# Kernel tuning notes

Measured on AMD Instinct MI355X. Metric: run time of the kernel, lower is better.

Reference implementation:

```python
import jax, jax.numpy as jnp
import numpy as np

B, L, T_BASE = 8192, 512, 4
T = T_BASE + 2            # +START, +STOP
START, STOP = T_BASE, T_BASE + 1
NEG = -10000.0


def setup_inputs() -> dict:
    key = jax.random.key(0)
    k1, k2, k3, k4 = jax.random.split(key, 4)
    feats = jax.random.normal(k1, (B, L, T), dtype=jnp.float32)
    trans = jax.random.normal(k2, (T, T), dtype=jnp.float32)
    # transitions[START, :] = -10000 (never transition out of nothing into START... i.e. into START)
    trans = trans.at[START, :].set(NEG)
    # transitions[:, STOP] = -10000 (never transition from STOP)
    trans = trans.at[:, STOP].set(NEG)
    tags = jax.random.randint(k3, (B, L), 0, T_BASE, dtype=jnp.int64)
    seq_lengths = jax.random.randint(k4, (B,), 1, L + 1, dtype=jnp.int32)
    return {"feats": feats, "transitions": trans, "tags": tags, "seq_lengths": seq_lengths}


def _crf_nll(feats, trans, tags, seq_lengths):
    # feats: [B, L, T], trans: [T, T] with trans[next, prev], tags: [B, L], seq_lengths: [B]
    mask = (jnp.arange(L)[None, :] < seq_lengths[:, None])  # [B, L] bool

    # ---- forward algorithm (log partition), batched over B, scanned over time ----
    init_alpha = jnp.full((feats.shape[0], T), NEG, dtype=feats.dtype).at[:, START].set(0.0)

    def step(alpha, xs):
        feat_t, mask_t = xs  # [B, T], [B]
        # scores[b, next, prev] = alpha[b, prev] + trans[next, prev]
        scores = alpha[:, None, :] + trans[None, :, :]
        new_alpha = jax.nn.logsumexp(scores, axis=-1) + feat_t  # [B, T]
        alpha = jnp.where(mask_t[:, None], new_alpha, alpha)
        return alpha, None

    feats_t = jnp.swapaxes(feats, 0, 1)   # [L, B, T]
    mask_t = jnp.swapaxes(mask, 0, 1)     # [L, B]
    alpha, _ = jax.lax.scan(step, init_alpha, (feats_t, mask_t))
    log_z = jax.nn.logsumexp(alpha + trans[STOP][None, :], axis=-1)  # [B]

    # ---- gold path score, fully vectorized ----
    tags32 = tags.astype(jnp.int32)
    start_col = jnp.full((tags32.shape[0], 1), START, dtype=jnp.int32)
    tags_ext = jnp.concatenate([start_col, tags32], axis=1)  # [B, L+1]
    trans_sc = trans[tags_ext[:, 1:], tags_ext[:, :-1]]       # [B, L]
    emit_sc = jnp.take_along_axis(feats, tags32[..., None], axis=2)[..., 0]  # [B, L]
    maskf = mask.astype(feats.dtype)
    gold = jnp.sum(maskf * (trans_sc + emit_sc), axis=1)      # [B]
    last_tag = jnp.take_along_axis(tags32, (seq_lengths[:, None] - 1).astype(jnp.int32), axis=1)[:, 0]
    gold = gold + trans[STOP, last_tag]

    return jnp.sum(log_z - gold) / feats.shape[0]


def reference(feats, transitions, tags, seq_lengths):
    return _crf_nll(feats, transitions, tags, seq_lengths)
```

## Files before the change

kernel.cpp:

```cpp
#include <hip/hip_runtime.h>


#define BB 8192
#define LL 512
#define LN2F 0.69314718055994530942f

__device__ __forceinline__ float uniformf(float x) {
    return __uint_as_float(__builtin_amdgcn_readfirstlane(__float_as_uint(x)));
}

#define RENORM16(P, MEX)                                                \
  do {                                                                  \
    float m_ = fmaxf(P[0], P[1]);                                       \
    _Pragma("unroll") for (int z_ = 2; z_ < 16; ++z_) m_ = fmaxf(m_, P[z_]); \
    const int ee_ = (int)((__float_as_uint(m_) >> 23) & 255) - 127;     \
    const float sc_ = __uint_as_float((unsigned)(127 - ee_) << 23);     \
    _Pragma("unroll") for (int z_ = 0; z_ < 16; ++z_) P[z_] *= sc_;     \
    MEX += ee_;                                                         \
  } while (0)

#define STEP(ABS, F0, F1, F2, F3, TG, PV)                               \
  do {                                                                  \
    const bool act_ = (ABS) < len;                                      \
    const float f0_=(F0), f1_=(F1), f2_=(F2), f3_=(F3);                 \
    const float fe0_=__expf(f0_), fe1_=__expf(f1_);                     \
    const float fe2_=__expf(f2_), fe3_=__expf(f3_);                     \
    _Pragma("unroll")                                                   \
    for (int j = 0; j < 4; ++j) {                                       \
      const float c0_=P[0*4+j], c1_=P[1*4+j], c2_=P[2*4+j], c3_=P[3*4+j]; \
      const float t0_ = fmaf(E[0], c0_, fmaf(E[1], c1_, fmaf(E[2], c2_, E[3] *c3_))); \
      const float t1_ = fmaf(E[4], c0_, fmaf(E[5], c1_, fmaf(E[6], c2_, E[7] *c3_))); \
      const float t2_ = fmaf(E[8], c0_, fmaf(E[9], c1_, fmaf(E[10],c2_, E[11]*c3_))); \
      const float t3_ = fmaf(E[12],c0_, fmaf(E[13],c1_, fmaf(E[14],c2_, E[15]*c3_))); \
      P[0*4+j] = act_ ? fe0_*t0_ : P[0*4+j];                            \
      P[1*4+j] = act_ ? fe1_*t1_ : P[1*4+j];                            \
      P[2*4+j] = act_ ? fe2_*t2_ : P[2*4+j];                            \
      P[3*4+j] = act_ ? fe3_*t3_ : P[3*4+j];                            \
    }                                                                   \
    const float lut_ = sT[(TG) * 6 + (PV)];                             \
    const float em_  = ((TG) & 2) ? (((TG) & 1) ? f3_ : f2_)            \
                                  : (((TG) & 1) ? f1_ : f0_);           \
    gold += act_ ? (lut_ + em_) : 0.f;                                  \
  } while (0)

#define TGAT(S)  ((int)((tpk >> (2*(S))) & 3u))
#define STEPE(S) STEP(base+(S), F0[(S)/2].x, F0[(S)/2].y, F0[(S)/2].z, F0[(S)/2].w, TGAT(S), TGAT((S)-1))
#define STEPO(S) STEP(base+(S), F1[(S)/2].x, F1[(S)/2].y, F2[(S)/2].x, F2[(S)/2].y, TGAT(S), TGAT((S)-1))

__global__ __launch_bounds__(256, 4) void crf_tree(
    const float* __restrict__ feats,
    const float* __restrict__ trans,
    const int*   __restrict__ tags,
    const int*   __restrict__ lens,
    float* __restrict__ partials)
{
    __shared__ float sT[36];

    const int tid  = threadIdx.x;
    const int lane = tid & 63;
    const int wv   = tid >> 6;
    const int g    = lane >> 5;
    const int c    = lane & 31;
    const int b    = blockIdx.x * 8 + wv * 2 + g;

    if (tid < 36) sT[tid] = trans[tid];
    __syncthreads();

    float E[16], e4[4], e5[4];
    #pragma unroll
    for (int i = 0; i < 16; ++i)
        E[i] = uniformf(__expf(sT[(i >> 2) * 6 + (i & 3)]));
    #pragma unroll
    for (int i = 0; i < 4; ++i) {
        e4[i] = uniformf(__expf(sT[i * 6 + 4]));
        e5[i] = uniformf(__expf(sT[30 + i]));
    }

    const int len  = lens[b];
    const int base = c * 16;
    const bool seg0 = (c == 0);

    const float* fp  = feats + (size_t)b * (LL * 6) + (size_t)base * 6;
    const int*   tbp = tags  + (size_t)b * LL + base;
    const int pv0 = seg0 ? 4 : (tbp[-1] & 3);

    float4 F0[8]; float2 F1[8], F2[8];
    #pragma unroll
    for (int p = 0; p < 8; ++p) {
        const float* q = fp + p * 12;
        F0[p] = *(const float4*)(q);
        F1[p] = *(const float2*)(q + 6);
        F2[p] = *(const float2*)(q + 8);
    }
    unsigned tpk = 0;
    #pragma unroll
    for (int q = 0; q < 4; ++q) {
        const int4 t = *(const int4*)(tbp + q * 4);
        tpk |= (unsigned)(t.x & 3) << (2*(q*4+0));
        tpk |= (unsigned)(t.y & 3) << (2*(q*4+1));
        tpk |= (unsigned)(t.z & 3) << (2*(q*4+2));
        tpk |= (unsigned)(t.w & 3) << (2*(q*4+3));
    }

    float P[16];
    #pragma unroll
    for (int z = 0; z < 16; ++z) P[z] = (z % 5 == 0) ? 1.f : 0.f;
    int   mex  = 0;
    float gold = 0.f;

    {
        const bool act_ = base < len;
        const float f0_=F0[0].x, f1_=F0[0].y, f2_=F0[0].z, f3_=F0[0].w;
        const float fe0_=__expf(f0_), fe1_=__expf(f1_);
        const float fe2_=__expf(f2_), fe3_=__expf(f3_);
        #pragma unroll
        for (int j = 0; j < 4; ++j) {
            const float u0 = seg0 ? e4[0] : E[0*4+j];
            const float u1 = seg0 ? e4[1] : E[1*4+j];
            const float u2 = seg0 ? e4[2] : E[2*4+j];
            const float u3 = seg0 ? e4[3] : E[3*4+j];
            P[0*4+j] = act_ ? fe0_*u0 : P[0*4+j];
            P[1*4+j] = act_ ? fe1_*u1 : P[1*4+j];
            P[2*4+j] = act_ ? fe2_*u2 : P[2*4+j];
            P[3*4+j] = act_ ? fe3_*u3 : P[3*4+j];
        }
        const int t0 = TGAT(0);
        const float lut_ = sT[t0 * 6 + pv0];
        const float em_  = (t0 & 2) ? ((t0 & 1) ? f3_ : f2_)
                                    : ((t0 & 1) ? f1_ : f0_);
        gold += act_ ? (lut_ + em_) : 0.f;
    }
    STEPO(1);  STEPE(2);  STEPO(3);  RENORM16(P, mex);
    STEPE(4);  STEPO(5);  STEPE(6);  STEPO(7);  RENORM16(P, mex);
    STEPE(8);  STEPO(9);  STEPE(10); STEPO(11); RENORM16(P, mex);
    STEPE(12); STEPO(13); STEPE(14); STEPO(15); RENORM16(P, mex);

    {
        const unsigned dl = (unsigned)(len - 1 - base);
        if (dl < 16u) gold += sT[30 + (int)((tpk >> (2*dl)) & 3u)];
    }

    #pragma unroll
    for (int k = 1; k <= 8; k <<= 1) {
        float Q[16];
        #pragma unroll
        for (int z = 0; z < 16; ++z) Q[z] = __shfl_down(P[z], k, 32);
        const int mq = __shfl_down(mex, k, 32);
        float N[16];
        #pragma unroll
        for (int i = 0; i < 4; ++i)
            #pragma unroll
            for (int j = 0; j < 4; ++j)
                N[i*4+j] = fmaf(Q[i*4+0], P[0*4+j], fmaf(Q[i*4+1], P[1*4+j],
                           fmaf(Q[i*4+2], P[2*4+j], Q[i*4+3] * P[3*4+j])));
        #pragma unroll
        for (int z = 0; z < 16; ++z) P[z] = N[z];
        mex += mq;
        if (k == 2 || k == 8) RENORM16(P, mex);
    }

    float al0, al1, al2, al3;
    {
        float Q[16];
        #pragma unroll
        for (int z = 0; z < 16; ++z) Q[z] = __shfl_down(P[z], 16, 32);
        const int mq = __shfl_down(mex, 16, 32);
        al0 = fmaf(Q[0], P[0], fmaf(Q[1], P[4], fmaf(Q[2], P[8], Q[3] *P[12])));
        al1 = fmaf(Q[4], P[0], fmaf(Q[5], P[4], fmaf(Q[6], P[8], Q[7] *P[12])));
        al2 = fmaf(Q[8], P[0], fmaf(Q[9], P[4], fmaf(Q[10],P[8], Q[11]*P[12])));
        al3 = fmaf(Q[12],P[0], fmaf(Q[13],P[4], fmaf(Q[14],P[8], Q[15]*P[12])));
        mex += mq;
    }

    #pragma unroll
    for (int k = 1; k <= 16; k <<= 1)
        gold += __shfl_xor(gold, k, 32);

    const float dot = fmaf(e5[0], al0, fmaf(e5[1], al1,
                      fmaf(e5[2], al2, e5[3] * al3)));
    const float logz = fmaf((float)mex, LN2F, __logf(dot));
    if (c == 0)
        partials[b] = logz - gold;
}

__global__ __launch_bounds__(256) void k_reduce(const float* __restrict__ partials,
                                               float* __restrict__ out)
{
    __shared__ float sh[256];
    const int t = threadIdx.x;
    float s = 0.f;
    #pragma unroll
    for (int j = 0; j < 32; ++j) s += partials[t + 256 * j];
    sh[t] = s;
    __syncthreads();
    #pragma unroll
    for (int d = 128; d > 0; d >>= 1) {
        if (t < d) sh[t] += sh[t + d];
        __syncthreads();
    }
    if (t == 0) out[0] = sh[0] * (1.0f / 8192.0f);
}

extern "C" void kernel_launch(void* const* d_in, const int* in_sizes, int n_in,
                              void* d_out, int out_size, void* d_ws, size_t ws_size,
                              hipStream_t stream) {
    const float* feats = (const float*)d_in[0];
    const float* trans = (const float*)d_in[1];
    const int*   tags  = (const int*)d_in[2];
    const int*   lens  = (const int*)d_in[3];
    float* out = (float*)d_out;
    float* partials = (float*)d_ws;

    crf_tree<<<BB / 8, 256, 0, stream>>>(feats, trans, tags, lens, partials);
    k_reduce<<<1, 256, 0, stream>>>(partials, out);
}
```

Before: 32.16 us.

## Size per-wave segment length to the wave's max sequence length

Each wave now sizes its segment length from the larger of its two sequences' lengths instead of a fixed 16 steps per lane. Feature and tag loads, and the scan steps beyond that length, are skipped behind wave-uniform guards. This cuts HBM traffic and ALU work for masked-out timesteps. The cost is extra branching and a less regular unrolled schedule, with renormalization now tied to the pair count.

After: 32.18 us. No clear change (+0.0%).

```diff
diff --git a/kernel.cpp b/kernel.cpp
--- a/kernel.cpp
+++ b/kernel.cpp
@@ -19,9 +19,9 @@
     MEX += ee_;                                                         \
   } while (0)
 
-#define STEP(ABS, F0, F1, F2, F3, TG, PV)                               \
+#define STEP(S, F0, F1, F2, F3, TG, PV)                                 \
   do {                                                                  \
-    const bool act_ = (ABS) < len;                                      \
+    const bool act_ = (base + (S)) < len;                               \
     const float f0_=(F0), f1_=(F1), f2_=(F2), f3_=(F3);                 \
     const float fe0_=__expf(f0_), fe1_=__expf(f1_);                     \
     const float fe2_=__expf(f2_), fe3_=__expf(f3_);                     \
@@ -44,8 +44,8 @@
   } while (0)
 
 #define TGAT(S)  ((int)((tpk >> (2*(S))) & 3u))
-#define STEPE(S) STEP(base+(S), F0[(S)/2].x, F0[(S)/2].y, F0[(S)/2].z, F0[(S)/2].w, TGAT(S), TGAT((S)-1))
-#define STEPO(S) STEP(base+(S), F1[(S)/2].x, F1[(S)/2].y, F2[(S)/2].x, F2[(S)/2].y, TGAT(S), TGAT((S)-1))
+#define STEPE(S) STEP((S), F0[(S)/2].x, F0[(S)/2].y, F0[(S)/2].z, F0[(S)/2].w, TGAT(S), TGAT((S)-1))
+#define STEPO(S) STEP((S), F1[(S)/2].x, F1[(S)/2].y, F2[(S)/2].x, F2[(S)/2].y, TGAT(S), TGAT((S)-1))
 
 __global__ __launch_bounds__(256, 4) void crf_tree(
     const float* __restrict__ feats,
@@ -76,8 +76,12 @@
         e5[i] = uniformf(__expf(sT[30 + i]));
     }
 
-    const int len  = lens[b];
-    const int base = c * 16;
+    const int len = lens[b];
+
+    const int wmax  = max(len, __shfl_xor(len, 32, 64));
+    const int seg2  = __builtin_amdgcn_readfirstlane(((wmax + 31) >> 5) + 1) & ~1;
+    const int npair = __builtin_amdgcn_readfirstlane(seg2 >> 1);
+    const int base  = c * seg2;
     const bool seg0 = (c == 0);
 
     const float* fp  = feats + (size_t)b * (LL * 6) + (size_t)base * 6;
@@ -86,21 +90,23 @@
 
     float4 F0[8]; float2 F1[8], F2[8];
     #pragma unroll
-    for (int p = 0; p < 8; ++p) {
-        const float* q = fp + p * 12;
-        F0[p] = *(const float4*)(q);
-        F1[p] = *(const float2*)(q + 6);
-        F2[p] = *(const float2*)(q + 8);
-    }
+    for (int p = 0; p < 8; ++p)
+        if (p < npair) {
+            const float* q = fp + p * 12;
+            F0[p] = *(const float4*)(q);
+            F1[p] = *(const float2*)(q + 6);
+            F2[p] = *(const float2*)(q + 8);
+        }
     unsigned tpk = 0;
     #pragma unroll
-    for (int q = 0; q < 4; ++q) {
-        const int4 t = *(const int4*)(tbp + q * 4);
-        tpk |= (unsigned)(t.x & 3) << (2*(q*4+0));
-        tpk |= (unsigned)(t.y & 3) << (2*(q*4+1));
-        tpk |= (unsigned)(t.z & 3) << (2*(q*4+2));
-        tpk |= (unsigned)(t.w & 3) << (2*(q*4+3));
-    }
+    for (int q = 0; q < 4; ++q)
+        if (q * 4 < seg2) {
+            const int4 t = *(const int4*)(tbp + q * 4);
+            tpk |= (unsigned)(t.x & 3) << (2*(q*4+0));
+            tpk |= (unsigned)(t.y & 3) << (2*(q*4+1));
+            tpk |= (unsigned)(t.z & 3) << (2*(q*4+2));
+            tpk |= (unsigned)(t.w & 3) << (2*(q*4+3));
+        }
 
     float P[16];
     #pragma unroll
@@ -129,15 +135,19 @@
         const float em_  = (t0 & 2) ? ((t0 & 1) ? f3_ : f2_)
                                     : ((t0 & 1) ? f1_ : f0_);
         gold += act_ ? (lut_ + em_) : 0.f;
-    }
-    STEPO(1);  STEPE(2);  STEPO(3);  RENORM16(P, mex);
-    STEPE(4);  STEPO(5);  STEPE(6);  STEPO(7);  RENORM16(P, mex);
-    STEPE(8);  STEPO(9);  STEPE(10); STEPO(11); RENORM16(P, mex);
-    STEPE(12); STEPO(13); STEPE(14); STEPO(15); RENORM16(P, mex);
+        STEPO(1);
+    }
+    if (npair > 1) { STEPE(2);  STEPO(3);  RENORM16(P, mex); }
+    if (npair > 2) { STEPE(4);  STEPO(5);  }
+    if (npair > 3) { STEPE(6);  STEPO(7);  RENORM16(P, mex); }
+    if (npair > 4) { STEPE(8);  STEPO(9);  }
+    if (npair > 5) { STEPE(10); STEPO(11); RENORM16(P, mex); }
+    if (npair > 6) { STEPE(12); STEPO(13); }
+    if (npair > 7) { STEPE(14); STEPO(15); RENORM16(P, mex); }
 
     {
         const unsigned dl = (unsigned)(len - 1 - base);
-        if (dl < 16u) gold += sT[30 + (int)((tpk >> (2*dl)) & 3u)];
+        if (dl < (unsigned)seg2) gold += sT[30 + (int)((tpk >> (2*dl)) & 3u)];
     }
 
     #pragma unroll
```
